# Performance work log

Measured on AMD Instinct MI355X. Metric: run time of the kernel, lower is better.

The kernel has to match this reference:

```python
import jax, jax.numpy as jnp
import numpy as np

B, N, D, E = 8, 512, 256, 16384  # batch, num_nodes, hidden_dim, num_edges


def setup_inputs() -> dict:
    key = jax.random.key(0)
    kf, ke, k1, k2, k3, k4 = jax.random.split(key, 6)
    features = jax.random.normal(kf, (B, N, D), dtype=jnp.float32)
    edge_index = jax.random.randint(ke, (2, E), 0, N, dtype=jnp.int64)
    # weight_net: Linear(2D -> D), ReLU, Linear(D -> 1), Sigmoid
    s1 = 1.0 / np.sqrt(2 * D)
    s2 = 1.0 / np.sqrt(D)
    W1 = jax.random.uniform(k1, (2 * D, D), jnp.float32, -s1, s1)
    b1 = jax.random.uniform(k2, (D,), jnp.float32, -s1, s1)
    W2 = jax.random.uniform(k3, (D, 1), jnp.float32, -s2, s2)
    b2 = jax.random.uniform(k4, (1,), jnp.float32, -s2, s2)
    return {"features": features, "W1": W1, "b1": b1, "W2": W2, "b2": b2,
            "edge_index": edge_index}


def reference(features, W1, b1, W2, b2, edge_index):
    src, dst = edge_index[0], edge_index[1]            # [E], [E]
    fi = features[:, src]                              # [B, E, D]
    fj = features[:, dst]                              # [B, E, D]
    pair = jnp.concatenate([fi, fj], axis=-1)          # [B, E, 2D]
    h = jax.nn.relu(jnp.einsum('bef,fh->beh', pair, W1) + b1)   # [B, E, D]
    s = jax.nn.sigmoid(jnp.einsum('beh,ho->beo', h, W2) + b2)[..., 0]  # [B, E]
    bsz, n = features.shape[0], features.shape[1]
    weights = jnp.zeros((bsz, n, n), features.dtype).at[:, src, dst].set(s)
    return weights
```

## Files before the change

kernel.cpp:

```cpp
#include <hip/hip_runtime.h>
#include <hip/hip_bf16.h>
#include <cstdint>

#define B_ 8
#define N_ 512
#define D_ 256
#define E_ 16384
#define H_ 256

#define SA_STRIDE 56
#define SB_STRIDE 56
#define BCAP 128

using bf16x8 = __attribute__((ext_vector_type(8))) short;
using f32x4  = __attribute__((ext_vector_type(4))) float;

__device__ inline unsigned short f2bf(float f) {
    union { float f; unsigned u; } v; v.f = f;
    unsigned u = v.u;
    return (unsigned short)((u + 0x7fffu + ((u >> 16) & 1u)) >> 16);
}

__global__ __launch_bounds__(256)
void prep_k(const float* __restrict__ W1, unsigned short* __restrict__ W1T,
            int* __restrict__ gCount) {
    __shared__ float tile[64][65];
    const int tb = blockIdx.x, t = threadIdx.x;
    if (tb == 32) {
        gCount[t] = 0;
        gCount[t + 256] = 0;
        return;
    }
    const int h   = tb >> 4;
    const int rem = tb & 15;
    const int tk  = (rem >> 2) * 64;
    const int tn  = (rem & 3) * 64;
    const float* Wh = W1 + (size_t)h * 256 * 256;
    const int c = t & 63, r0 = t >> 6;
#pragma unroll
    for (int i = 0; i < 16; i++) {
        int r = r0 + i * 4;
        tile[r][c] = Wh[(size_t)(tk + r) * 256 + tn + c];
    }
    __syncthreads();
#pragma unroll
    for (int i = 0; i < 16; i++) {
        int rn = r0 + i * 4;
        W1T[(size_t)(h * 256 + tn + rn) * 256 + tk + c] = f2bf(tile[c][rn]);
    }
}

__global__ __launch_bounds__(256)
void node_gemm(const float* __restrict__ feat,
               const unsigned short* __restrict__ W1T,
               const float* __restrict__ b1,
               const int* __restrict__ eidx,
               unsigned short* __restrict__ P,
               float4* __restrict__ out4,
               int* __restrict__ gCount, int* __restrict__ gBucket) {
    const int t = threadIdx.x;

    if (blockIdx.x >= 128) {
        __shared__ int hist[512];
        __shared__ int base[512];
        const int sb = blockIdx.x - 128;
        int mysrc[8], mydst[8], myslot[8];
        for (int i = t; i < 512; i += 256) hist[i] = 0;
        __syncthreads();
#pragma unroll
        for (int i = 0; i < 8; i++) {
            int e = sb * 2048 + i * 256 + t;
            mysrc[i] = eidx[e];
            mydst[i] = eidx[E_ + e];
            myslot[i] = atomicAdd(&hist[mysrc[i]], 1);
        }
        __syncthreads();
        for (int i = t; i < 512; i += 256) {
            int c = hist[i];
            base[i] = c ? atomicAdd(&gCount[i], c) : 0;
        }
        __syncthreads();
#pragma unroll
        for (int i = 0; i < 8; i++)
            gBucket[(mysrc[i] << 7) + base[mysrc[i]] + myslot[i]] = mydst[i];
        return;
    }

    __shared__ unsigned short sA[64 * SA_STRIDE];
    __shared__ unsigned short sB[256 * SB_STRIDE];

    const int bm = blockIdx.x >> 1;
    const int bn = blockIdx.x & 1;
    const int m0 = bm * 64;

    {
        float4 z = make_float4(0.f, 0.f, 0.f, 0.f);
        float4* oz = out4 + (size_t)blockIdx.x * 4096 + t;
#pragma unroll
        for (int i = 0; i < 16; i++) oz[i * 256] = z;
    }

    const int arow = t >> 2;
    const int akg  = (t & 3) * 8;
    const float* pA = feat + (size_t)(m0 + arow) * 256;
    const unsigned short* pB = W1T + (size_t)(bn * 256 + t) * 256;

    const int wave = t >> 6, lane = t & 63, l15 = lane & 15, quad = lane >> 4;

    f32x4 acc[4][4];
#pragma unroll
    for (int rm = 0; rm < 4; rm++)
#pragma unroll
        for (int cn = 0; cn < 4; cn++)
            acc[rm][cn] = (f32x4){0.f, 0.f, 0.f, 0.f};

    for (int k0 = 0; k0 < 256; k0 += 32) {
        __syncthreads();
        {
            float4 lo = *(const float4*)(pA + k0 + akg);
            float4 hi = *(const float4*)(pA + k0 + akg + 4);
            union { bf16x8 v; unsigned short s[8]; } u;
            u.s[0] = f2bf(lo.x); u.s[1] = f2bf(lo.y); u.s[2] = f2bf(lo.z); u.s[3] = f2bf(lo.w);
            u.s[4] = f2bf(hi.x); u.s[5] = f2bf(hi.y); u.s[6] = f2bf(hi.z); u.s[7] = f2bf(hi.w);
            *(bf16x8*)(sA + arow * SA_STRIDE + akg) = u.v;
        }
        {
            const unsigned short* p = pB + k0;
            uint4 q0 = *(const uint4*)(p);
            uint4 q1 = *(const uint4*)(p + 8);
            uint4 q2 = *(const uint4*)(p + 16);
            uint4 q3 = *(const uint4*)(p + 24);
            *(uint4*)(sB + t * SB_STRIDE +  0) = q0;
            *(uint4*)(sB + t * SB_STRIDE +  8) = q1;
            *(uint4*)(sB + t * SB_STRIDE + 16) = q2;
            *(uint4*)(sB + t * SB_STRIDE + 24) = q3;
        }
        __syncthreads();

        bf16x8 af[4], bfr[4];
#pragma unroll
        for (int rm = 0; rm < 4; rm++)
            af[rm] = *(const bf16x8*)(sA + (rm * 16 + l15) * SA_STRIDE + quad * 8);
#pragma unroll
        for (int cn = 0; cn < 4; cn++)
            bfr[cn] = *(const bf16x8*)(sB + (wave * 64 + cn * 16 + l15) * SB_STRIDE + quad * 8);
#pragma unroll
        for (int rm = 0; rm < 4; rm++)
#pragma unroll
            for (int cn = 0; cn < 4; cn++)
                acc[rm][cn] = __builtin_amdgcn_mfma_f32_16x16x32_bf16(af[rm], bfr[cn], acc[rm][cn], 0, 0, 0);
    }

#pragma unroll
    for (int cn = 0; cn < 4; cn++) {
        int colh = wave * 64 + cn * 16 + l15;
        float bias = (bn == 0) ? b1[colh] : 0.f;
        int col = bn * 256 + colh;
#pragma unroll
        for (int rm = 0; rm < 4; rm++)
#pragma unroll
            for (int r = 0; r < 4; r++) {
                int row = m0 + rm * 16 + quad * 4 + r;
                P[(size_t)row * 512 + col] = f2bf(acc[rm][cn][r] + bias);
            }
    }
}

__device__ inline float dot8nb(uint4 qu, uint4 qv, const float* w2p) {
    unsigned us[4] = {qu.x, qu.y, qu.z, qu.w};
    unsigned vs[4] = {qv.x, qv.y, qv.z, qv.w};
    float p = 0.f;
#pragma unroll
    for (int j = 0; j < 4; j++) {
        float ulo = __uint_as_float(us[j] << 16);
        float uhi = __uint_as_float(us[j] & 0xffff0000u);
        float vlo = __uint_as_float(vs[j] << 16);
        float vhi = __uint_as_float(vs[j] & 0xffff0000u);
        float hlo = fmaxf(ulo + vlo, 0.f);
        float hhi = fmaxf(uhi + vhi, 0.f);
        p = fmaf(hlo, w2p[2 * j],     p);
        p = fmaf(hhi, w2p[2 * j + 1], p);
    }
    return p;
}

__global__ __launch_bounds__(256)
void edge_score(const unsigned short* __restrict__ P,
                const float* __restrict__ W2, const float* __restrict__ b2,
                const int* __restrict__ gCount, const int* __restrict__ gBucket,
                float* __restrict__ out) {
    const int b     = blockIdx.x & 7;
    const int chunk = blockIdx.x >> 3;
    const int lane  = threadIdx.x & 63;
    const int wave  = threadIdx.x >> 6;
    const int g     = lane >> 4;
    const int w     = lane & 15;
    const int wid   = wave * 4 + g;
    const int s     = 2 * chunk + (wid >> 3);
    const int o     = wid & 7;

    const int en = gCount[s];
    const int* bucket = gBucket + (s << 7);

    float w2r[16];
#pragma unroll
    for (int j = 0; j < 4; j++)
        *(float4*)(w2r + 4 * j) = *(const float4*)(W2 + w * 16 + 4 * j);
    const float b2v = b2[0];

    const unsigned short* Pu = P + ((size_t)b * 512 + s) * 512 + w * 16;
    uint4 u0 = *(const uint4*)(Pu);
    uint4 u1 = *(const uint4*)(Pu + 8);
    const unsigned short* Pv = P + (size_t)b * 512 * 512 + 256 + w * 16;
    float* outb = out + ((size_t)b * 512 + s) * 512;

    int j = o;
    int dst0 = 0; uint4 v00 = {}, v01 = {};
    if (j < en) {
        dst0 = bucket[j];
        const unsigned short* pv = Pv + (size_t)dst0 * 512;
        v00 = *(const uint4*)pv; v01 = *(const uint4*)(pv + 8);
    }
    while (j < en) {
        int jn = j + 8;
        int dst1 = 0; uint4 v10 = {}, v11 = {};
        if (jn < en) {
            dst1 = bucket[jn];
            const unsigned short* pv = Pv + (size_t)dst1 * 512;
            v10 = *(const uint4*)pv; v11 = *(const uint4*)(pv + 8);
        }
        float p = dot8nb(u0, v00, w2r) + dot8nb(u1, v01, w2r + 8);
        p += __shfl_xor(p, 1);
        p += __shfl_xor(p, 2);
        p += __shfl_xor(p, 4);
        p += __shfl_xor(p, 8);
        if (w == 0) {
            float sv = 1.0f / (1.0f + __expf(-(p + b2v)));
            outb[dst0] = sv;
        }
        dst0 = dst1; v00 = v10; v01 = v11; j = jn;
    }
}

extern "C" void kernel_launch(void* const* d_in, const int* in_sizes, int n_in,
                              void* d_out, int out_size, void* d_ws, size_t ws_size,
                              hipStream_t stream) {
    const float* feat = (const float*)d_in[0];
    const float* W1   = (const float*)d_in[1];
    const float* b1   = (const float*)d_in[2];
    const float* W2   = (const float*)d_in[3];
    const float* b2   = (const float*)d_in[4];
    const int*   eidx = (const int*)d_in[5];
    float* out = (float*)d_out;

    unsigned short* W1T = (unsigned short*)d_ws;
    unsigned short* P   = (unsigned short*)((char*)d_ws + (1 << 20));
    int* gCount  = (int*)((char*)d_ws + (6 << 20));
    int* gBucket = (int*)((char*)d_ws + (6 << 20) + 4096);

    prep_k<<<33, 256, 0, stream>>>(W1, W1T, gCount);
    node_gemm<<<136, 256, 0, stream>>>(feat, W1T, b1, eidx, P, (float4*)out, gCount, gBucket);
    edge_score<<<2048, 256, 0, stream>>>(P, W2, b2, gCount, gBucket, out);
}
```

Before: 92.27 us.

## Halve node GEMM tile rows and move edge bucketing into prep kernel

The node GEMM block tile drops from 64 to 32 rows, so the grid grows from 128 to 256 GEMM blocks and covers more of the GPU's compute units. Edge bucketing by source node moves out of the GEMM kernel into the W1 transpose/prep kernel, and counter zeroing gets its own tiny kernel. The aim is to balance the GEMM launch and hide the bucketing work behind the weight transpose. In exchange it adds an extra kernel launch, and each B tile loaded into shared memory is reused over fewer rows.

```diff
diff --git a/kernel.cpp b/kernel.cpp
--- a/kernel.cpp
+++ b/kernel.cpp
@@ -10,9 +10,9 @@
 
 #define SA_STRIDE 56
 #define SB_STRIDE 56
-#define BCAP 128
 
 using bf16x8 = __attribute__((ext_vector_type(8))) short;
+using bf16x4 = __attribute__((ext_vector_type(4))) short;
 using f32x4  = __attribute__((ext_vector_type(4))) float;
 
 __device__ inline unsigned short f2bf(float f) {
@@ -22,15 +22,44 @@
 }
 
 __global__ __launch_bounds__(256)
-void prep_k(const float* __restrict__ W1, unsigned short* __restrict__ W1T,
-            int* __restrict__ gCount) {
+void zero_cnt(int* __restrict__ gCount) {
+    gCount[threadIdx.x] = 0;
+    gCount[threadIdx.x + 256] = 0;
+}
+
+__global__ __launch_bounds__(256)
+void prep_k(const float* __restrict__ W1, const int* __restrict__ eidx,
+            unsigned short* __restrict__ W1T,
+            int* __restrict__ gCount, int* __restrict__ gBucket) {
+    const int tb = blockIdx.x, t = threadIdx.x;
+
+    if (tb >= 32) {
+        __shared__ int hist[512];
+        __shared__ int base[512];
+        const int sb = tb - 32;
+        int mysrc[8], mydst[8], myslot[8];
+        for (int i = t; i < 512; i += 256) hist[i] = 0;
+        __syncthreads();
+#pragma unroll
+        for (int i = 0; i < 8; i++) {
+            int e = sb * 2048 + i * 256 + t;
+            mysrc[i] = eidx[e];
+            mydst[i] = eidx[E_ + e];
+            myslot[i] = atomicAdd(&hist[mysrc[i]], 1);
+        }
+        __syncthreads();
+        for (int i = t; i < 512; i += 256) {
+            int c = hist[i];
+            base[i] = c ? atomicAdd(&gCount[i], c) : 0;
+        }
+        __syncthreads();
+#pragma unroll
+        for (int i = 0; i < 8; i++)
+            gBucket[(mysrc[i] << 7) + base[mysrc[i]] + myslot[i]] = mydst[i];
+        return;
+    }
+
     __shared__ float tile[64][65];
-    const int tb = blockIdx.x, t = threadIdx.x;
-    if (tb == 32) {
-        gCount[t] = 0;
-        gCount[t + 256] = 0;
-        return;
-    }
     const int h   = tb >> 4;
     const int rem = tb & 15;
     const int tk  = (rem >> 2) * 64;
@@ -54,62 +83,33 @@
 void node_gemm(const float* __restrict__ feat,
                const unsigned short* __restrict__ W1T,
                const float* __restrict__ b1,
-               const int* __restrict__ eidx,
                unsigned short* __restrict__ P,
-               float4* __restrict__ out4,
-               int* __restrict__ gCount, int* __restrict__ gBucket) {
-    const int t = threadIdx.x;
-
-    if (blockIdx.x >= 128) {
-        __shared__ int hist[512];
-        __shared__ int base[512];
-        const int sb = blockIdx.x - 128;
-        int mysrc[8], mydst[8], myslot[8];
-        for (int i = t; i < 512; i += 256) hist[i] = 0;
-        __syncthreads();
-#pragma unroll
-        for (int i = 0; i < 8; i++) {
-            int e = sb * 2048 + i * 256 + t;
-            mysrc[i] = eidx[e];
-            mydst[i] = eidx[E_ + e];
-            myslot[i] = atomicAdd(&hist[mysrc[i]], 1);
-        }
-        __syncthreads();
-        for (int i = t; i < 512; i += 256) {
-            int c = hist[i];
-            base[i] = c ? atomicAdd(&gCount[i], c) : 0;
-        }
-        __syncthreads();
-#pragma unroll
-        for (int i = 0; i < 8; i++)
-            gBucket[(mysrc[i] << 7) + base[mysrc[i]] + myslot[i]] = mydst[i];
-        return;
-    }
-
-    __shared__ unsigned short sA[64 * SA_STRIDE];
+               float4* __restrict__ out4) {
+    __shared__ unsigned short sA[32 * SA_STRIDE];
     __shared__ unsigned short sB[256 * SB_STRIDE];
 
+    const int t  = threadIdx.x;
     const int bm = blockIdx.x >> 1;
     const int bn = blockIdx.x & 1;
-    const int m0 = bm * 64;
+    const int m0 = bm * 32;
 
     {
         float4 z = make_float4(0.f, 0.f, 0.f, 0.f);
-        float4* oz = out4 + (size_t)blockIdx.x * 4096 + t;
-#pragma unroll
-        for (int i = 0; i < 16; i++) oz[i * 256] = z;
-    }
-
-    const int arow = t >> 2;
-    const int akg  = (t & 3) * 8;
+        float4* oz = out4 + (size_t)blockIdx.x * 2048 + t;
+#pragma unroll
+        for (int i = 0; i < 8; i++) oz[i * 256] = z;
+    }
+
+    const int arow = t >> 3;
+    const int akg  = (t & 7) * 4;
     const float* pA = feat + (size_t)(m0 + arow) * 256;
     const unsigned short* pB = W1T + (size_t)(bn * 256 + t) * 256;
 
     const int wave = t >> 6, lane = t & 63, l15 = lane & 15, quad = lane >> 4;
 
-    f32x4 acc[4][4];
-#pragma unroll
-    for (int rm = 0; rm < 4; rm++)
+    f32x4 acc[2][4];
+#pragma unroll
+    for (int rm = 0; rm < 2; rm++)
 #pragma unroll
         for (int cn = 0; cn < 4; cn++)
             acc[rm][cn] = (f32x4){0.f, 0.f, 0.f, 0.f};
@@ -118,11 +118,10 @@
         __syncthreads();
         {
             float4 lo = *(const float4*)(pA + k0 + akg);
-            float4 hi = *(const float4*)(pA + k0 + akg + 4);
-            union { bf16x8 v; unsigned short s[8]; } u;
-            u.s[0] = f2bf(lo.x); u.s[1] = f2bf(lo.y); u.s[2] = f2bf(lo.z); u.s[3] = f2bf(lo.w);
-            u.s[4] = f2bf(hi.x); u.s[5] = f2bf(hi.y); u.s[6] = f2bf(hi.z); u.s[7] = f2bf(hi.w);
-            *(bf16x8*)(sA + arow * SA_STRIDE + akg) = u.v;
+            union { bf16x4 v; unsigned short s[4]; } u;
+            u.s[0] = f2bf(lo.x); u.s[1] = f2bf(lo.y);
+            u.s[2] = f2bf(lo.z); u.s[3] = f2bf(lo.w);
+            *(bf16x4*)(sA + arow * SA_STRIDE + akg) = u.v;
         }
         {
             const unsigned short* p = pB + k0;
@@ -137,15 +136,15 @@
         }
         __syncthreads();
 
-        bf16x8 af[4], bfr[4];
-#pragma unroll
-        for (int rm = 0; rm < 4; rm++)
+        bf16x8 af[2], bfr[4];
+#pragma unroll
+        for (int rm = 0; rm < 2; rm++)
             af[rm] = *(const bf16x8*)(sA + (rm * 16 + l15) * SA_STRIDE + quad * 8);
 #pragma unroll
         for (int cn = 0; cn < 4; cn++)
             bfr[cn] = *(const bf16x8*)(sB + (wave * 64 + cn * 16 + l15) * SB_STRIDE + quad * 8);
 #pragma unroll
-        for (int rm = 0; rm < 4; rm++)
+        for (int rm = 0; rm < 2; rm++)
 #pragma unroll
             for (int cn = 0; cn < 4; cn++)
                 acc[rm][cn] = __builtin_amdgcn_mfma_f32_16x16x32_bf16(af[rm], bfr[cn], acc[rm][cn], 0, 0, 0);
@@ -157,7 +156,7 @@
         float bias = (bn == 0) ? b1[colh] : 0.f;
         int col = bn * 256 + colh;
 #pragma unroll
-        for (int rm = 0; rm < 4; rm++)
+        for (int rm = 0; rm < 2; rm++)
 #pragma unroll
             for (int r = 0; r < 4; r++) {
                 int row = m0 + rm * 16 + quad * 4 + r;
@@ -258,7 +257,8 @@
     int* gCount  = (int*)((char*)d_ws + (6 << 20));
     int* gBucket = (int*)((char*)d_ws + (6 << 20) + 4096);
 
-    prep_k<<<33, 256, 0, stream>>>(W1, W1T, gCount);
-    node_gemm<<<136, 256, 0, stream>>>(feat, W1T, b1, eidx, P, (float4*)out, gCount, gBucket);
+    zero_cnt<<<1, 256, 0, stream>>>(gCount);
+    prep_k<<<40, 256, 0, stream>>>(W1, eidx, W1T, gCount, gBucket);
+    node_gemm<<<256, 256, 0, stream>>>(feat, W1T, b1, P, (float4*)out);
     edge_score<<<2048, 256, 0, stream>>>(P, W2, b2, gCount, gBucket, out);
 }
```

Result: slower. 94.64 us (+2.6%).
